# Kernel optimization log

Measured on AMD Instinct MI355X. Metric: run time of the kernel, lower is better.

Reference implementation:

```python
import jax, jax.numpy as jnp
from jax import lax
import numpy as np

T = 36
N_POLES = 161
GAMMA = 0.05
MAX_ITER = 40


def creat_real_dictionary(T, rr, theta):
    # i = 0..T-1 power/frequency index
    i = jnp.arange(T, dtype=rr.dtype)[:, None]            # [T,1]
    ri = rr[None, :] ** i                                  # rr^i, [T,N]
    sgn = jnp.where(jnp.arange(T)[:, None] % 2 == 0, 1.0, -1.0).astype(rr.dtype)
    nri = sgn * ri                                         # (-rr)^i
    c = jnp.cos(i * theta[None, :])
    s = jnp.sin(i * theta[None, :])
    ones = jnp.ones((T, 1), rr.dtype)
    dic = jnp.concatenate([ones, ri * c, nri * c, ri * s, nri * s], axis=1)  # [T, 4N+1]
    G = jnp.linalg.norm(dic, axis=0)                       # column norms
    G = jnp.where(G == 0, jnp.sqrt(jnp.asarray(T, rr.dtype)), G)
    return dic / G


def fista(D, Y, gamma, max_iter):
    DtD = D.T @ D                                          # [K,K]
    L = jnp.linalg.norm(DtD)                               # Frobenius norm (torch.norm(., p=2))
    linv = jnp.where(L == 0, 0.0, 1.0 / L)
    DtY = jnp.einsum('tk,btp->bkp', D, Y) * linv           # [B,K,P]
    lambd = gamma * linv                                   # scalar
    A = jnp.eye(DtD.shape[0], dtype=D.dtype) - DtD * linv  # [K,K]

    # momentum coefficients are data-independent -> precompute on host
    t = 1.0
    tts = []
    for _ in range(max_iter):
        t_new = (1 + np.sqrt(1 + 4 * t * t)) / 2.0
        tts.append((t - 1) / t_new)
        t = t_new
    tts = jnp.asarray(np.asarray(tts, dtype=np.float32))

    x0 = jnp.zeros(DtY.shape, dtype=D.dtype)

    def step(carry, tt):
        x_old, y_old = carry
        Ay = jnp.einsum('kj,bjp->bkp', A, y_old)
        x_new = Ay + DtY - lambd
        # faithful to source: sign(x) * max(|x|, 0)
        x_new = jnp.sign(x_new) * jnp.maximum(jnp.abs(x_new), 0.0)
        y_new = x_new * (1 + tt) - x_old * tt
        return (x_new, y_new), None

    (x_final, _), _ = lax.scan(step, (x0, x0), tts)
    return x_final


def setup_inputs() -> dict:
    key = jax.random.key(0)
    k1, k2, k3 = jax.random.split(key, 3)
    B, P = 1, 8192
    x = jax.random.normal(k1, (B, T, P), dtype=jnp.float32)
    # pole radii near unit circle, angles in [0, pi]
    rr = 0.85 + 0.3 * jax.random.uniform(k2, (N_POLES,), dtype=jnp.float32)
    theta = np.pi * jax.random.uniform(k3, (N_POLES,), dtype=jnp.float32)
    return {"x": x, "rr": rr, "theta": theta}


def reference(x, rr, theta):
    dic = creat_real_dictionary(T, rr, theta)
    return fista(dic, x, GAMMA, MAX_ITER)
```

## Files before the change

kernel.cpp:

```cpp
#include <hip/hip_runtime.h>
#include <math.h>

#define T36   36
#define NPOLE 161
#define K645  645
#define KH    37
#define NITER 40
#define GAMMA_C 0.05


__global__ void k_build(const float* __restrict__ rr, const float* __restrict__ theta,
                        double* __restrict__ Di) {
    int k = blockIdx.x * blockDim.x + threadIdx.x;
    if (k >= K645) return;
    if (k == 0) {
        const double inv = 1.0 / 6.0;
#pragma unroll
        for (int i = 0; i < T36; ++i) Di[i * K645] = inv;
        return;
    }
    int g = (k - 1) / NPOLE;
    int p = (k - 1) % NPOLE;
    double r  = (double)rr[p];
    double th = (double)theta[p];
    bool alt     = (g == 1) || (g == 3);
    bool use_sin = (g >= 2);
    double sth, cth;
    sincos(th, &sth, &cth);
    double ci = 1.0, si = 0.0, rp = 1.0, ss = 0.0;
    double val[T36];
#pragma unroll
    for (int i = 0; i < T36; ++i) {
        double v = rp * (use_sin ? si : ci);
        if (alt && (i & 1)) v = -v;
        val[i] = v;
        ss += v * v;
        double cn = ci * cth - si * sth;
        double sn = si * cth + ci * sth;
        ci = cn; si = sn; rp *= r;
    }
    double gn = sqrt(ss);
    if (gn == 0.0) gn = 6.0;
    double inv = 1.0 / gn;
#pragma unroll
    for (int i = 0; i < T36; ++i) Di[i * K645 + k] = val[i] * inv;
}

__global__ __launch_bounds__(64) void k_gram(const double* __restrict__ Di,
                                             double* __restrict__ G36,
                                             double* __restrict__ d1v) {
    int a = blockIdx.x;
    int b = blockIdx.y;
    int lane = threadIdx.x;
    const double* Da = Di + a * K645;
    double acc = 0.0;
    if (b < T36) {
        const double* Db = Di + b * K645;
        for (int k = lane; k < K645; k += 64) acc += Da[k] * Db[k];
    } else {
        for (int k = lane; k < K645; k += 64) acc += Da[k];
    }
#pragma unroll
    for (int off = 32; off > 0; off >>= 1) acc += __shfl_down(acc, off);
    if (lane == 0) {
        if (b < T36) G36[a * T36 + b] = acc;
        else         d1v[a] = acc;
    }
}

__global__ __launch_bounds__(64) void k_solve(const double* __restrict__ Di,
                                              const double* __restrict__ G36,
                                              const double* __restrict__ d1v,
                                              float* __restrict__ Mf) {
    int t = blockIdx.x;
    int lane = threadIdx.x;
    double s = 0.0;
    for (int i = lane; i < T36 * T36; i += 64) { double v = G36[i]; s += v * v; }
#pragma unroll
    for (int off = 32; off > 0; off >>= 1) s += __shfl_xor(s, off);
    double L = sqrt(s);
    double linv = (L == 0.0) ? 0.0 : 1.0 / L;
    double lambd = GAMMA_C * linv;

    double Hreg[KH];
    double Eh = 0.0, xold = 0.0;
    __shared__ double yl[KH];
    __shared__ double xl[KH];
    if (lane < KH) {
        if (lane < T36) {
#pragma unroll
            for (int q = 0; q < T36; ++q)
                Hreg[q] = ((lane == q) ? 1.0 : 0.0) - linv * G36[lane * T36 + q];
            Hreg[T36] = -linv * d1v[lane];
            Eh = (lane == t && t < T36) ? linv : 0.0;
        } else {
#pragma unroll
            for (int q = 0; q < KH; ++q) Hreg[q] = (q == T36) ? 1.0 : 0.0;
            Eh = (t == T36) ? -lambd : 0.0;
        }
        yl[lane] = 0.0;
    } else {
#pragma unroll
        for (int q = 0; q < KH; ++q) Hreg[q] = 0.0;
    }
    __syncthreads();
    double tcur = 1.0;
    for (int n = 0; n < NITER; ++n) {
        double tn = 0.5 * (1.0 + sqrt(1.0 + 4.0 * tcur * tcur));
        double tt = (double)(float)((tcur - 1.0) / tn);
        tcur = tn;
        double a0 = Eh, a1 = 0.0;
#pragma unroll
        for (int q = 0; q < T36; q += 2) {
            a0 += Hreg[q] * yl[q];
            a1 += Hreg[q + 1] * yl[q + 1];
        }
        double acc = a0 + a1 + Hreg[T36] * yl[T36];
        __syncthreads();
        double ynew = (1.0 + tt) * acc - tt * xold;
        xold = acc;
        if (lane < KH) yl[lane] = ynew;
        __syncthreads();
    }
    if (lane < KH) xl[lane] = xold;
    __syncthreads();
    for (int k = lane; k < K645; k += 64) {
        double acc = xl[T36];
#pragma unroll
        for (int q = 0; q < T36; ++q) acc += Di[q * K645 + k] * xl[q];
        Mf[k * KH + t] = (float)acc;
    }
}

__global__ __launch_bounds__(256) void k_out(const float* __restrict__ Y,
                                             const float* __restrict__ Mf,
                                             float* __restrict__ out, int P) {
    int p = blockIdx.x * 256 + threadIdx.x;
    if (p >= P) return;
    int k0 = blockIdx.y * 15;
    float y[T36];
#pragma unroll
    for (int t = 0; t < T36; ++t) y[t] = Y[t * P + p];
    for (int kk = 0; kk < 15; ++kk) {
        int k = k0 + kk;
        const float* m = Mf + k * KH;
        float acc = m[T36];
#pragma unroll
        for (int t = 0; t < T36; ++t) acc = fmaf(m[t], y[t], acc);
        out[k * P + p] = acc;
    }
}

extern "C" void kernel_launch(void* const* d_in, const int* in_sizes, int n_in,
                              void* d_out, int out_size, void* d_ws, size_t ws_size,
                              hipStream_t stream) {
    const float* x     = (const float*)d_in[0];
    const float* rr    = (const float*)d_in[1];
    const float* theta = (const float*)d_in[2];
    float* out = (float*)d_out;

    double* ws   = (double*)d_ws;
    double* Di   = ws;
    double* G36  = ws + 23220;
    double* d1v  = ws + 24516;
    float*  Mf   = (float*)(ws + 24552);

    int P = in_sizes[0] / T36;

    k_build<<<dim3((K645 + 255) / 256), dim3(256), 0, stream>>>(rr, theta, Di);
    k_gram<<<dim3(T36, KH), dim3(64), 0, stream>>>(Di, G36, d1v);
    k_solve<<<dim3(KH), dim3(64), 0, stream>>>(Di, G36, d1v, Mf);
    k_out<<<dim3((P + 255) / 256, 43), dim3(256), 0, stream>>>(x, Mf, out, P);
}
```

Baseline: 110.4 us.

## Store dictionary in fp32 padded layout and use shuffles in solve loop

Switches the dictionary, Gram matrix and bias vector from double to float, with rows padded to 648 so the Gram kernel can use float4 loads. The FISTA iteration loop in k_solve now broadcasts y through wavefront shuffles instead of shared memory, removing two barriers per iteration, and the final projection runs in float. The aim is to cut latency in the small setup kernels, at the cost of lower precision in the Gram matrix and the projection.

```diff
diff --git a/kernel.cpp b/kernel.cpp
--- a/kernel.cpp
+++ b/kernel.cpp
@@ -4,19 +4,25 @@
 #define T36   36
 #define NPOLE 161
 #define K645  645
+#define KP    648
 #define KH    37
 #define NITER 40
 #define GAMMA_C 0.05
 
 
 __global__ void k_build(const float* __restrict__ rr, const float* __restrict__ theta,
-                        double* __restrict__ Di) {
+                        float* __restrict__ Dif) {
     int k = blockIdx.x * blockDim.x + threadIdx.x;
-    if (k >= K645) return;
+    if (k >= KP) return;
+    if (k >= K645) {
+#pragma unroll
+        for (int i = 0; i < T36; ++i) Dif[i * KP + k] = 0.f;
+        return;
+    }
     if (k == 0) {
-        const double inv = 1.0 / 6.0;
+        const float inv = 1.0f / 6.0f;
 #pragma unroll
-        for (int i = 0; i < T36; ++i) Di[i * K645] = inv;
+        for (int i = 0; i < T36; ++i) Dif[i * KP] = inv;
         return;
     }
     int g = (k - 1) / NPOLE;
@@ -43,39 +49,47 @@
     if (gn == 0.0) gn = 6.0;
     double inv = 1.0 / gn;
 #pragma unroll
-    for (int i = 0; i < T36; ++i) Di[i * K645 + k] = val[i] * inv;
+    for (int i = 0; i < T36; ++i) Dif[i * KP + k] = (float)(val[i] * inv);
 }
 
-__global__ __launch_bounds__(64) void k_gram(const double* __restrict__ Di,
-                                             double* __restrict__ G36,
-                                             double* __restrict__ d1v) {
+__global__ __launch_bounds__(64) void k_gram(const float* __restrict__ Dif,
+                                             float* __restrict__ G36,
+                                             float* __restrict__ d1v) {
     int a = blockIdx.x;
     int b = blockIdx.y;
     int lane = threadIdx.x;
-    const double* Da = Di + a * K645;
-    double acc = 0.0;
+    const float4* Da = (const float4*)(Dif + a * KP);
+    float4 acc4 = make_float4(0.f, 0.f, 0.f, 0.f);
     if (b < T36) {
-        const double* Db = Di + b * K645;
-        for (int k = lane; k < K645; k += 64) acc += Da[k] * Db[k];
+        const float4* Db = (const float4*)(Dif + b * KP);
+        for (int c = lane; c < KP / 4; c += 64) {
+            float4 va = Da[c], vb = Db[c];
+            acc4.x += va.x * vb.x; acc4.y += va.y * vb.y;
+            acc4.z += va.z * vb.z; acc4.w += va.w * vb.w;
+        }
     } else {
-        for (int k = lane; k < K645; k += 64) acc += Da[k];
+        for (int c = lane; c < KP / 4; c += 64) {
+            float4 va = Da[c];
+            acc4.x += va.x; acc4.y += va.y; acc4.z += va.z; acc4.w += va.w;
+        }
     }
+    float acc = (acc4.x + acc4.y) + (acc4.z + acc4.w);
 #pragma unroll
-    for (int off = 32; off > 0; off >>= 1) acc += __shfl_down(acc, off);
+    for (int off = 32; off > 0; off >>= 1) acc += __shfl_xor(acc, off);
     if (lane == 0) {
         if (b < T36) G36[a * T36 + b] = acc;
         else         d1v[a] = acc;
     }
 }
 
-__global__ __launch_bounds__(64) void k_solve(const double* __restrict__ Di,
-                                              const double* __restrict__ G36,
-                                              const double* __restrict__ d1v,
+__global__ __launch_bounds__(64) void k_solve(const float* __restrict__ Dif,
+                                              const float* __restrict__ G36,
+                                              const float* __restrict__ d1v,
                                               float* __restrict__ Mf) {
     int t = blockIdx.x;
     int lane = threadIdx.x;
     double s = 0.0;
-    for (int i = lane; i < T36 * T36; i += 64) { double v = G36[i]; s += v * v; }
+    for (int i = lane; i < T36 * T36; i += 64) { double v = (double)G36[i]; s += v * v; }
 #pragma unroll
     for (int off = 32; off > 0; off >>= 1) s += __shfl_xor(s, off);
     double L = sqrt(s);
@@ -83,52 +97,52 @@
     double lambd = GAMMA_C * linv;
 
     double Hreg[KH];
-    double Eh = 0.0, xold = 0.0;
-    __shared__ double yl[KH];
-    __shared__ double xl[KH];
-    if (lane < KH) {
-        if (lane < T36) {
+    double Eh = 0.0;
+    if (lane < T36) {
 #pragma unroll
-            for (int q = 0; q < T36; ++q)
-                Hreg[q] = ((lane == q) ? 1.0 : 0.0) - linv * G36[lane * T36 + q];
-            Hreg[T36] = -linv * d1v[lane];
-            Eh = (lane == t && t < T36) ? linv : 0.0;
-        } else {
+        for (int q = 0; q < T36; ++q)
+            Hreg[q] = ((lane == q) ? 1.0 : 0.0) - linv * (double)G36[lane * T36 + q];
+        Hreg[T36] = -linv * (double)d1v[lane];
+        Eh = (lane == t && t < T36) ? linv : 0.0;
+    } else if (lane == T36) {
 #pragma unroll
-            for (int q = 0; q < KH; ++q) Hreg[q] = (q == T36) ? 1.0 : 0.0;
-            Eh = (t == T36) ? -lambd : 0.0;
-        }
-        yl[lane] = 0.0;
+        for (int q = 0; q < KH; ++q) Hreg[q] = (q == T36) ? 1.0 : 0.0;
+        Eh = (t == T36) ? -lambd : 0.0;
     } else {
 #pragma unroll
         for (int q = 0; q < KH; ++q) Hreg[q] = 0.0;
     }
-    __syncthreads();
+    double y = 0.0, xold = 0.0;
     double tcur = 1.0;
     for (int n = 0; n < NITER; ++n) {
         double tn = 0.5 * (1.0 + sqrt(1.0 + 4.0 * tcur * tcur));
         double tt = (double)(float)((tcur - 1.0) / tn);
         tcur = tn;
-        double a0 = Eh, a1 = 0.0;
+        double a0 = Eh, a1 = 0.0, a2 = 0.0, a3 = 0.0;
 #pragma unroll
-        for (int q = 0; q < T36; q += 2) {
-            a0 += Hreg[q] * yl[q];
-            a1 += Hreg[q + 1] * yl[q + 1];
+        for (int q = 0; q < T36; q += 4) {
+            a0 += Hreg[q]     * __shfl(y, q);
+            a1 += Hreg[q + 1] * __shfl(y, q + 1);
+            a2 += Hreg[q + 2] * __shfl(y, q + 2);
+            a3 += Hreg[q + 3] * __shfl(y, q + 3);
         }
-        double acc = a0 + a1 + Hreg[T36] * yl[T36];
-        __syncthreads();
+        a0 += Hreg[T36] * __shfl(y, T36);
+        double acc = (a0 + a1) + (a2 + a3);
         double ynew = (1.0 + tt) * acc - tt * xold;
         xold = acc;
-        if (lane < KH) yl[lane] = ynew;
-        __syncthreads();
+        y = ynew;
     }
-    if (lane < KH) xl[lane] = xold;
+    __shared__ float xs[KH];
+    if (lane < KH) xs[lane] = (float)xold;
     __syncthreads();
+    float xr[KH];
+#pragma unroll
+    for (int q = 0; q < KH; ++q) xr[q] = xs[q];
     for (int k = lane; k < K645; k += 64) {
-        double acc = xl[T36];
+        float acc = xr[T36];
 #pragma unroll
-        for (int q = 0; q < T36; ++q) acc += Di[q * K645 + k] * xl[q];
-        Mf[k * KH + t] = (float)acc;
+        for (int q = 0; q < T36; ++q) acc += Dif[q * KP + k] * xr[q];
+        Mf[k * KH + t] = acc;
     }
 }
 
@@ -159,16 +173,16 @@
     const float* theta = (const float*)d_in[2];
     float* out = (float*)d_out;
 
-    double* ws   = (double*)d_ws;
-    double* Di   = ws;
-    double* G36  = ws + 23220;
-    double* d1v  = ws + 24516;
-    float*  Mf   = (float*)(ws + 24552);
+    float* wsf = (float*)d_ws;
+    float* Dif = wsf;
+    float* G36 = wsf + 23328;
+    float* d1v = wsf + 24624;
+    float* Mf  = wsf + 24660;
 
     int P = in_sizes[0] / T36;
 
-    k_build<<<dim3((K645 + 255) / 256), dim3(256), 0, stream>>>(rr, theta, Di);
-    k_gram<<<dim3(T36, KH), dim3(64), 0, stream>>>(Di, G36, d1v);
-    k_solve<<<dim3(KH), dim3(64), 0, stream>>>(Di, G36, d1v, Mf);
+    k_build<<<dim3(3), dim3(256), 0, stream>>>(rr, theta, Dif);
+    k_gram<<<dim3(T36, KH), dim3(64), 0, stream>>>(Dif, G36, d1v);
+    k_solve<<<dim3(KH), dim3(64), 0, stream>>>(Dif, G36, d1v, Mf);
     k_out<<<dim3((P + 255) / 256, 43), dim3(256), 0, stream>>>(x, Mf, out, P);
 }
```

Result: slower. 142.8 us (+29.3%).
